# Kernel optimization log

Hardware: AMD Instinct MI355X
Metric: run time of the kernel (lower is better)

## Reference

```python
import jax, jax.numpy as jnp
import numpy as np

B_, N, C = 4096, 49, 128
H = 4          # num_heads
NW = 64        # windows per image


def setup_inputs() -> dict:
    key = jax.random.key(0)
    k = jax.random.split(key, 6)
    s = 0.02
    return {
        "x": jax.random.normal(k[0], (B_, N, C), jnp.float32),
        "mask": jax.random.normal(k[1], (NW, N, N), jnp.float32),
        "qkv_w": jax.random.normal(k[2], (3 * C, C), jnp.float32) * s,
        "qkv_b": jax.random.normal(k[3], (3 * C,), jnp.float32) * s,
        "proj_w": jax.random.normal(k[4], (C, C), jnp.float32) * s,
        "proj_b": jax.random.normal(k[5], (C,), jnp.float32) * s,
    }


def reference(x, mask, qkv_w, qkv_b, proj_w, proj_b):
    b, n, c = x.shape
    hd = c // H
    scale = hd ** -0.5
    # fused QKV projection: [b, n, 3, H, hd] -> [3, b, H, n, hd]
    qkv = (x @ qkv_w.T + qkv_b).reshape(b, n, 3, H, hd)
    qkv = jnp.transpose(qkv, (2, 0, 3, 1, 4))
    q, k, v = qkv[0] * scale, qkv[1], qkv[2]
    attn = jnp.einsum("bhnd,bhmd->bhnm", q, k)  # [b, H, n, n]
    nW = mask.shape[0]
    attn = attn.reshape(b // nW, nW, H, n, n) + mask[None, :, None, :, :]
    attn = jax.nn.softmax(attn.reshape(b, H, n, n), axis=-1)
    out = jnp.einsum("bhnm,bhmd->bhnd", attn, v)
    out = jnp.transpose(out, (0, 2, 1, 3)).reshape(b, n, c)
    return out @ proj_w.T + proj_b
```

## Files before the change

### kernel.cpp

```cpp
#include <hip/hip_runtime.h>
#include <hip/hip_bf16.h>

#define N_TOK 49
#define C_DIM 128
#define HD 32
#define SCALE 0.17677669529663687f

typedef __attribute__((ext_vector_type(8))) short frag8;
typedef __attribute__((ext_vector_type(4))) float f32x4;

#define XBF_OFF 0
#define XBF_STR 136
#define MSK_OFF 8704
#define MSK_STR 52
#define HEAD_OFF 11264
#define HEAD_SZ 7424
#define Q_STR 40
#define VT_STR 72
#define P_STR 72
#define SMEM_TOT 40960

__device__ __forceinline__ unsigned short f2b(float x) {
    __hip_bfloat16 h = __float2bfloat16(x);
    return __builtin_bit_cast(unsigned short, h);
}
__device__ __forceinline__ float b2f(unsigned short u) {
    return __builtin_bit_cast(float, (unsigned)u << 16);
}

__global__ void convert_weights(const float* __restrict__ qkvw,
                                const float* __restrict__ projw,
                                unsigned short* __restrict__ wbf) {
    int i = blockIdx.x * 256 + threadIdx.x;
    float v = (i < 49152) ? qkvw[i] : projw[i - 49152];
    wbf[i] = f2b(v);
}

__global__ __launch_bounds__(256) void attn_mfma(
    const float* __restrict__ x,
    const float* __restrict__ mask,
    const float* __restrict__ qkv_b,
    const float* __restrict__ proj_b,
    const unsigned short* __restrict__ wq,
    float* __restrict__ out)
{
    __shared__ __align__(16) unsigned short sm[SMEM_TOT];

    const int b = blockIdx.x, tid = threadIdx.x;
    const int w = tid >> 6;
    const int lane = tid & 63;
    const int n16 = lane & 15;
    const int q = lane >> 4;

    {
        const float4* xg = (const float4*)(x + (size_t)b * 6272);
        for (int i = tid; i < 1568; i += 256) {
            float4 v = xg[i];
            int row = i >> 5, col = (i & 31) << 2;
            ushort4 pk;
            pk.x = f2b(v.x); pk.y = f2b(v.y); pk.z = f2b(v.z); pk.w = f2b(v.w);
            *(ushort4*)&sm[XBF_OFF + row * XBF_STR + col] = pk;
        }
        for (int i = tid; i < 15 * XBF_STR; i += 256)
            sm[XBF_OFF + 49 * XBF_STR + i] = 0;
        const float* mg = mask + (size_t)(b & 63) * 2401;
        for (int i = tid; i < 2401; i += 256) {
            int r = i / 49, c = i - r * 49;
            sm[MSK_OFF + r * MSK_STR + c] = f2b(mg[i]);
        }
    }
    __syncthreads();

    const int Qb = HEAD_OFF + w * HEAD_SZ;
    const int Kb = Qb + 2560;
    const int Vb = Qb + 5120;
    const int Pb = Qb;

    frag8 a[4][4];
#pragma unroll
    for (int mt = 0; mt < 4; ++mt)
#pragma unroll
        for (int ks = 0; ks < 4; ++ks)
            a[mt][ks] = *(const frag8*)&sm[XBF_OFF + (mt * 16 + n16) * XBF_STR + ks * 32 + q * 8];

#pragma unroll
    for (int mat = 0; mat < 3; ++mat) {
#pragma unroll
        for (int nt = 0; nt < 2; ++nt) {
            const unsigned short* wrow = wq + (size_t)(mat * C_DIM + w * HD + nt * 16 + n16) * C_DIM;
            frag8 bf[4];
#pragma unroll
            for (int ks = 0; ks < 4; ++ks) bf[ks] = *(const frag8*)(wrow + ks * 32 + q * 8);
            float bias = qkv_b[mat * C_DIM + w * HD + nt * 16 + n16];
#pragma unroll
            for (int mt = 0; mt < 4; ++mt) {
                f32x4 acc = {0.f, 0.f, 0.f, 0.f};
#pragma unroll
                for (int ks = 0; ks < 4; ++ks)
                    acc = __builtin_amdgcn_mfma_f32_16x16x32_bf16(a[mt][ks], bf[ks], acc, 0, 0, 0);
                if (mat == 2) {
                    ushort4 pk;
                    pk.x = f2b(acc[0] + bias); pk.y = f2b(acc[1] + bias);
                    pk.z = f2b(acc[2] + bias); pk.w = f2b(acc[3] + bias);
                    *(ushort4*)&sm[Vb + (nt * 16 + n16) * VT_STR + mt * 16 + q * 4] = pk;
                } else {
                    const int base = (mat == 0) ? Qb : Kb;
                    const float sc = (mat == 0) ? SCALE : 1.f;
#pragma unroll
                    for (int r = 0; r < 4; ++r)
                        sm[base + (mt * 16 + q * 4 + r) * Q_STR + nt * 16 + n16] =
                            f2b((acc[r] + bias) * sc);
                }
            }
        }
    }

    frag8 qf[4], kf[4];
#pragma unroll
    for (int t = 0; t < 4; ++t) {
        qf[t] = *(const frag8*)&sm[Qb + (t * 16 + n16) * Q_STR + q * 8];
        kf[t] = *(const frag8*)&sm[Kb + (t * 16 + n16) * Q_STR + q * 8];
    }
    f32x4 s[4][4];
#pragma unroll
    for (int mt = 0; mt < 4; ++mt)
#pragma unroll
        for (int nt = 0; nt < 4; ++nt) {
            int cc = min(nt * 16 + n16, 48);
#pragma unroll
            for (int r = 0; r < 4; ++r) {
                int rc = min(mt * 16 + q * 4 + r, 48);
                s[mt][nt][r] = b2f(sm[MSK_OFF + rc * MSK_STR + cc]);
            }
            s[mt][nt] = __builtin_amdgcn_mfma_f32_16x16x32_bf16(qf[mt], kf[nt], s[mt][nt], 0, 0, 0);
        }

#pragma unroll
    for (int mt = 0; mt < 4; ++mt) {
#pragma unroll
        for (int r = 0; r < 4; ++r) {
            float mx = -1e30f;
#pragma unroll
            for (int nt = 0; nt < 4; ++nt)
                if (nt * 16 + n16 < 49) mx = fmaxf(mx, s[mt][nt][r]);
#pragma unroll
            for (int d = 1; d < 16; d <<= 1) mx = fmaxf(mx, __shfl_xor(mx, d));
            float sum = 0.f;
#pragma unroll
            for (int nt = 0; nt < 4; ++nt) {
                float e = (nt * 16 + n16 < 49) ? __expf(s[mt][nt][r] - mx) : 0.f;
                s[mt][nt][r] = e;
                sum += e;
            }
#pragma unroll
            for (int d = 1; d < 16; d <<= 1) sum += __shfl_xor(sum, d);
            float inv = __builtin_amdgcn_rcpf(sum);
#pragma unroll
            for (int nt = 0; nt < 4; ++nt) s[mt][nt][r] *= inv;
        }
    }

#pragma unroll
    for (int mt = 0; mt < 4; ++mt)
#pragma unroll
        for (int nt = 0; nt < 4; ++nt)
#pragma unroll
            for (int r = 0; r < 4; ++r)
                sm[Pb + (mt * 16 + q * 4 + r) * P_STR + nt * 16 + n16] = f2b(s[mt][nt][r]);

    frag8 vf[2][2];
#pragma unroll
    for (int nt = 0; nt < 2; ++nt)
#pragma unroll
        for (int ks = 0; ks < 2; ++ks)
            vf[nt][ks] = *(const frag8*)&sm[Vb + (nt * 16 + n16) * VT_STR + ks * 32 + q * 8];
    f32x4 o[4][2];
#pragma unroll
    for (int mt = 0; mt < 4; ++mt)
#pragma unroll
        for (int nt = 0; nt < 2; ++nt) o[mt][nt] = (f32x4){0.f, 0.f, 0.f, 0.f};
#pragma unroll
    for (int mt = 0; mt < 4; ++mt)
#pragma unroll
        for (int ks = 0; ks < 2; ++ks) {
            frag8 pf = *(const frag8*)&sm[Pb + (mt * 16 + n16) * P_STR + ks * 32 + q * 8];
#pragma unroll
            for (int nt = 0; nt < 2; ++nt)
                o[mt][nt] = __builtin_amdgcn_mfma_f32_16x16x32_bf16(pf, vf[nt][ks], o[mt][nt], 0, 0, 0);
        }

    __syncthreads();
#pragma unroll
    for (int mt = 0; mt < 4; ++mt)
#pragma unroll
        for (int nt = 0; nt < 2; ++nt)
#pragma unroll
            for (int r = 0; r < 4; ++r)
                sm[XBF_OFF + (mt * 16 + q * 4 + r) * XBF_STR + w * HD + nt * 16 + n16] =
                    f2b(o[mt][nt][r]);
    __syncthreads();

    frag8 af[4][4];
#pragma unroll
    for (int mt = 0; mt < 4; ++mt)
#pragma unroll
        for (int ks = 0; ks < 4; ++ks)
            af[mt][ks] = *(const frag8*)&sm[XBF_OFF + (mt * 16 + n16) * XBF_STR + ks * 32 + q * 8];

    const unsigned short* pw = wq + 49152;
    float* outb = out + (size_t)b * 6272;
#pragma unroll
    for (int nt = 0; nt < 2; ++nt) {
        const unsigned short* wrow = pw + (size_t)(w * HD + nt * 16 + n16) * C_DIM;
        frag8 bf[4];
#pragma unroll
        for (int ks = 0; ks < 4; ++ks) bf[ks] = *(const frag8*)(wrow + ks * 32 + q * 8);
        float bias = proj_b[w * HD + nt * 16 + n16];
#pragma unroll
        for (int mt = 0; mt < 4; ++mt) {
            f32x4 acc = {0.f, 0.f, 0.f, 0.f};
#pragma unroll
            for (int ks = 0; ks < 4; ++ks)
                acc = __builtin_amdgcn_mfma_f32_16x16x32_bf16(af[mt][ks], bf[ks], acc, 0, 0, 0);
#pragma unroll
            for (int r = 0; r < 4; ++r) {
                int row = mt * 16 + q * 4 + r;
                if (row < 49) outb[row * C_DIM + w * HD + nt * 16 + n16] = acc[r] + bias;
            }
        }
    }
}

extern "C" void kernel_launch(void* const* d_in, const int* in_sizes, int n_in,
                              void* d_out, int out_size, void* d_ws, size_t ws_size,
                              hipStream_t stream) {
    const float* x      = (const float*)d_in[0];
    const float* mask   = (const float*)d_in[1];
    const float* qkv_w  = (const float*)d_in[2];
    const float* qkv_b  = (const float*)d_in[3];
    const float* proj_w = (const float*)d_in[4];
    const float* proj_b = (const float*)d_in[5];

    unsigned short* wbf = (unsigned short*)d_ws;
    convert_weights<<<256, 256, 0, stream>>>(qkv_w, proj_w, wbf);
    attn_mfma<<<4096, 256, 0, stream>>>(x, mask, qkv_b, proj_b, wbf, (float*)d_out);
}
```

Measured before the change: 305.8 us.

## Split each head across two waves with 512-thread blocks; vectorize weight conversion

The attention kernel now runs 8 waves per block instead of 4. Two waves share each head, and each wave handles half of the 16-row M tiles for the QKV projection, scores, softmax and PV. In the output projection each wave owns 16 output columns. Extra block barriers are added because waves now read K/V tiles written by their partner wave, and P overwrites the Q region. The weight-conversion kernel is also vectorized to float4/ushort4 with fewer blocks. The goal is more latency hiding and parallelism per block, at the cost of more barriers and duplicated weight-fragment loads.

```diff
diff --git a/kernel.cpp b/kernel.cpp
--- a/kernel.cpp
+++ b/kernel.cpp
@@ -1,7 +1,6 @@
 #include <hip/hip_runtime.h>
 #include <hip/hip_bf16.h>
 
-#define N_TOK 49
 #define C_DIM 128
 #define HD 32
 #define SCALE 0.17677669529663687f
@@ -28,15 +27,17 @@
     return __builtin_bit_cast(float, (unsigned)u << 16);
 }
 
-__global__ void convert_weights(const float* __restrict__ qkvw,
-                                const float* __restrict__ projw,
-                                unsigned short* __restrict__ wbf) {
+__global__ void convert_weights(const float4* __restrict__ qkvw,
+                                const float4* __restrict__ projw,
+                                ushort4* __restrict__ wbf) {
     int i = blockIdx.x * 256 + threadIdx.x;
-    float v = (i < 49152) ? qkvw[i] : projw[i - 49152];
-    wbf[i] = f2b(v);
-}
-
-__global__ __launch_bounds__(256) void attn_mfma(
+    float4 v = (i < 12288) ? qkvw[i] : projw[i - 12288];
+    ushort4 p;
+    p.x = f2b(v.x); p.y = f2b(v.y); p.z = f2b(v.z); p.w = f2b(v.w);
+    wbf[i] = p;
+}
+
+__global__ __launch_bounds__(512, 4) void attn_mfma(
     const float* __restrict__ x,
     const float* __restrict__ mask,
     const float* __restrict__ qkv_b,
@@ -47,53 +48,56 @@
     __shared__ __align__(16) unsigned short sm[SMEM_TOT];
 
     const int b = blockIdx.x, tid = threadIdx.x;
-    const int w = tid >> 6;
+    const int wave = tid >> 6;
+    const int h    = wave >> 1;
+    const int half = wave & 1;
     const int lane = tid & 63;
-    const int n16 = lane & 15;
-    const int q = lane >> 4;
+    const int n16  = lane & 15;
+    const int q    = lane >> 4;
 
     {
         const float4* xg = (const float4*)(x + (size_t)b * 6272);
-        for (int i = tid; i < 1568; i += 256) {
+        for (int i = tid; i < 1568; i += 512) {
             float4 v = xg[i];
             int row = i >> 5, col = (i & 31) << 2;
             ushort4 pk;
             pk.x = f2b(v.x); pk.y = f2b(v.y); pk.z = f2b(v.z); pk.w = f2b(v.w);
             *(ushort4*)&sm[XBF_OFF + row * XBF_STR + col] = pk;
         }
-        for (int i = tid; i < 15 * XBF_STR; i += 256)
+        for (int i = tid; i < 15 * XBF_STR; i += 512)
             sm[XBF_OFF + 49 * XBF_STR + i] = 0;
         const float* mg = mask + (size_t)(b & 63) * 2401;
-        for (int i = tid; i < 2401; i += 256) {
+        for (int i = tid; i < 2401; i += 512) {
             int r = i / 49, c = i - r * 49;
             sm[MSK_OFF + r * MSK_STR + c] = f2b(mg[i]);
         }
     }
     __syncthreads();
 
-    const int Qb = HEAD_OFF + w * HEAD_SZ;
+    const int Qb = HEAD_OFF + h * HEAD_SZ;
     const int Kb = Qb + 2560;
     const int Vb = Qb + 5120;
     const int Pb = Qb;
 
-    frag8 a[4][4];
-#pragma unroll
-    for (int mt = 0; mt < 4; ++mt)
+    frag8 a[2][4];
+#pragma unroll
+    for (int mt = 0; mt < 2; ++mt)
 #pragma unroll
         for (int ks = 0; ks < 4; ++ks)
-            a[mt][ks] = *(const frag8*)&sm[XBF_OFF + (mt * 16 + n16) * XBF_STR + ks * 32 + q * 8];
+            a[mt][ks] = *(const frag8*)&sm[XBF_OFF + ((half * 2 + mt) * 16 + n16) * XBF_STR + ks * 32 + q * 8];
 
 #pragma unroll
     for (int mat = 0; mat < 3; ++mat) {
 #pragma unroll
         for (int nt = 0; nt < 2; ++nt) {
-            const unsigned short* wrow = wq + (size_t)(mat * C_DIM + w * HD + nt * 16 + n16) * C_DIM;
+            const unsigned short* wrow = wq + (size_t)(mat * C_DIM + h * HD + nt * 16 + n16) * C_DIM;
             frag8 bf[4];
 #pragma unroll
             for (int ks = 0; ks < 4; ++ks) bf[ks] = *(const frag8*)(wrow + ks * 32 + q * 8);
-            float bias = qkv_b[mat * C_DIM + w * HD + nt * 16 + n16];
-#pragma unroll
-            for (int mt = 0; mt < 4; ++mt) {
+            float bias = qkv_b[mat * C_DIM + h * HD + nt * 16 + n16];
+#pragma unroll
+            for (int mt = 0; mt < 2; ++mt) {
+                const int gm = half * 2 + mt;
                 f32x4 acc = {0.f, 0.f, 0.f, 0.f};
 #pragma unroll
                 for (int ks = 0; ks < 4; ++ks)
@@ -102,41 +106,44 @@
                     ushort4 pk;
                     pk.x = f2b(acc[0] + bias); pk.y = f2b(acc[1] + bias);
                     pk.z = f2b(acc[2] + bias); pk.w = f2b(acc[3] + bias);
-                    *(ushort4*)&sm[Vb + (nt * 16 + n16) * VT_STR + mt * 16 + q * 4] = pk;
+                    *(ushort4*)&sm[Vb + (nt * 16 + n16) * VT_STR + gm * 16 + q * 4] = pk;
                 } else {
                     const int base = (mat == 0) ? Qb : Kb;
                     const float sc = (mat == 0) ? SCALE : 1.f;
 #pragma unroll
                     for (int r = 0; r < 4; ++r)
-                        sm[base + (mt * 16 + q * 4 + r) * Q_STR + nt * 16 + n16] =
+                        sm[base + (gm * 16 + q * 4 + r) * Q_STR + nt * 16 + n16] =
                             f2b((acc[r] + bias) * sc);
                 }
             }
         }
     }
-
-    frag8 qf[4], kf[4];
-#pragma unroll
-    for (int t = 0; t < 4; ++t) {
-        qf[t] = *(const frag8*)&sm[Qb + (t * 16 + n16) * Q_STR + q * 8];
+    __syncthreads();
+
+    frag8 qf[2], kf[4];
+#pragma unroll
+    for (int mt = 0; mt < 2; ++mt)
+        qf[mt] = *(const frag8*)&sm[Qb + ((half * 2 + mt) * 16 + n16) * Q_STR + q * 8];
+#pragma unroll
+    for (int t = 0; t < 4; ++t)
         kf[t] = *(const frag8*)&sm[Kb + (t * 16 + n16) * Q_STR + q * 8];
-    }
-    f32x4 s[4][4];
-#pragma unroll
-    for (int mt = 0; mt < 4; ++mt)
+
+    f32x4 s[2][4];
+#pragma unroll
+    for (int mt = 0; mt < 2; ++mt)
 #pragma unroll
         for (int nt = 0; nt < 4; ++nt) {
             int cc = min(nt * 16 + n16, 48);
 #pragma unroll
             for (int r = 0; r < 4; ++r) {
-                int rc = min(mt * 16 + q * 4 + r, 48);
+                int rc = min((half * 2 + mt) * 16 + q * 4 + r, 48);
                 s[mt][nt][r] = b2f(sm[MSK_OFF + rc * MSK_STR + cc]);
             }
             s[mt][nt] = __builtin_amdgcn_mfma_f32_16x16x32_bf16(qf[mt], kf[nt], s[mt][nt], 0, 0, 0);
         }
 
 #pragma unroll
-    for (int mt = 0; mt < 4; ++mt) {
+    for (int mt = 0; mt < 2; ++mt) {
 #pragma unroll
         for (int r = 0; r < 4; ++r) {
             float mx = -1e30f;
@@ -159,14 +166,16 @@
             for (int nt = 0; nt < 4; ++nt) s[mt][nt][r] *= inv;
         }
     }
-
-#pragma unroll
-    for (int mt = 0; mt < 4; ++mt)
+    __syncthreads();
+
+#pragma unroll
+    for (int mt = 0; mt < 2; ++mt)
 #pragma unroll
         for (int nt = 0; nt < 4; ++nt)
 #pragma unroll
             for (int r = 0; r < 4; ++r)
-                sm[Pb + (mt * 16 + q * 4 + r) * P_STR + nt * 16 + n16] = f2b(s[mt][nt][r]);
+                sm[Pb + ((half * 2 + mt) * 16 + q * 4 + r) * P_STR + nt * 16 + n16] =
+                    f2b(s[mt][nt][r]);
 
     frag8 vf[2][2];
 #pragma unroll
@@ -174,29 +183,28 @@
 #pragma unroll
         for (int ks = 0; ks < 2; ++ks)
             vf[nt][ks] = *(const frag8*)&sm[Vb + (nt * 16 + n16) * VT_STR + ks * 32 + q * 8];
-    f32x4 o[4][2];
-#pragma unroll
-    for (int mt = 0; mt < 4; ++mt)
+    f32x4 o[2][2];
+#pragma unroll
+    for (int mt = 0; mt < 2; ++mt)
 #pragma unroll
         for (int nt = 0; nt < 2; ++nt) o[mt][nt] = (f32x4){0.f, 0.f, 0.f, 0.f};
 #pragma unroll
-    for (int mt = 0; mt < 4; ++mt)
+    for (int mt = 0; mt < 2; ++mt)
 #pragma unroll
         for (int ks = 0; ks < 2; ++ks) {
-            frag8 pf = *(const frag8*)&sm[Pb + (mt * 16 + n16) * P_STR + ks * 32 + q * 8];
+            frag8 pf = *(const frag8*)&sm[Pb + ((half * 2 + mt) * 16 + n16) * P_STR + ks * 32 + q * 8];
 #pragma unroll
             for (int nt = 0; nt < 2; ++nt)
                 o[mt][nt] = __builtin_amdgcn_mfma_f32_16x16x32_bf16(pf, vf[nt][ks], o[mt][nt], 0, 0, 0);
         }
 
-    __syncthreads();
-#pragma unroll
-    for (int mt = 0; mt < 4; ++mt)
+#pragma unroll
+    for (int mt = 0; mt < 2; ++mt)
 #pragma unroll
         for (int nt = 0; nt < 2; ++nt)
 #pragma unroll
             for (int r = 0; r < 4; ++r)
-                sm[XBF_OFF + (mt * 16 + q * 4 + r) * XBF_STR + w * HD + nt * 16 + n16] =
+                sm[XBF_OFF + ((half * 2 + mt) * 16 + q * 4 + r) * XBF_STR + h * HD + nt * 16 + n16] =
                     f2b(o[mt][nt][r]);
     __syncthreads();
 
@@ -209,13 +217,12 @@
 
     const unsigned short* pw = wq + 49152;
     float* outb = out + (size_t)b * 6272;
-#pragma unroll
-    for (int nt = 0; nt < 2; ++nt) {
-        const unsigned short* wrow = pw + (size_t)(w * HD + nt * 16 + n16) * C_DIM;
+    {
+        const unsigned short* wrow = pw + (size_t)(wave * 16 + n16) * C_DIM;
         frag8 bf[4];
 #pragma unroll
         for (int ks = 0; ks < 4; ++ks) bf[ks] = *(const frag8*)(wrow + ks * 32 + q * 8);
-        float bias = proj_b[w * HD + nt * 16 + n16];
+        float bias = proj_b[wave * 16 + n16];
 #pragma unroll
         for (int mt = 0; mt < 4; ++mt) {
             f32x4 acc = {0.f, 0.f, 0.f, 0.f};
@@ -225,7 +232,7 @@
 #pragma unroll
             for (int r = 0; r < 4; ++r) {
                 int row = mt * 16 + q * 4 + r;
-                if (row < 49) outb[row * C_DIM + w * HD + nt * 16 + n16] = acc[r] + bias;
+                if (row < 49) outb[row * C_DIM + wave * 16 + n16] = acc[r] + bias;
             }
         }
     }
@@ -236,12 +243,12 @@
                               hipStream_t stream) {
     const float* x      = (const float*)d_in[0];
     const float* mask   = (const float*)d_in[1];
-    const float* qkv_w  = (const float*)d_in[2];
     const float* qkv_b  = (const float*)d_in[3];
-    const float* proj_w = (const float*)d_in[4];
     const float* proj_b = (const float*)d_in[5];
 
     unsigned short* wbf = (unsigned short*)d_ws;
-    convert_weights<<<256, 256, 0, stream>>>(qkv_w, proj_w, wbf);
-    attn_mfma<<<4096, 256, 0, stream>>>(x, mask, qkv_b, proj_b, wbf, (float*)d_out);
-}
+    convert_weights<<<64, 256, 0, stream>>>((const float4*)d_in[2],
+                                            (const float4*)d_in[4],
+                                            (ushort4*)wbf);
+    attn_mfma<<<4096, 512, 0, stream>>>(x, mask, qkv_b, proj_b, wbf, (float*)d_out);
+}
```

New measurement: 294.3 us. 1.04x faster.
